# Optimization experiments

Hardware: AMD Instinct MI355X
Metric: run time of the kernel (lower is better)

Reference implementation:

```python
import jax, jax.numpy as jnp
import numpy as np

_FRAC_BITS = 8  # assumed fixed-point fractional bits for bits_quant
_SCALE = float(2 ** _FRAC_BITS)

def bits_quant(x):
    # Simulated fixed-point quantization: round to nearest multiple of 2^-8.
    return jnp.round(x * _SCALE) / _SCALE


def setup_inputs() -> dict:
    key = jax.random.key(0)
    k1, k2, k3 = jax.random.split(key, 3)
    B, D_in, D_out = 4096, 4096, 4096
    inputs = jax.random.normal(k1, (B, D_in), dtype=jnp.float32)
    w = jax.random.normal(k2, (D_in, D_out), dtype=jnp.float32) * 0.02
    b = jax.random.normal(k3, (D_out,), dtype=jnp.float32) * 0.02
    return {"inputs": inputs, "w": w, "b": b}


def reference(inputs, w, b):
    # y = bits_quant(inputs @ w) + bits_quant(b); out = bits_quant(y)
    y = bits_quant(jnp.matmul(inputs, w)) + bits_quant(b)
    return bits_quant(y)
```

## Files before the change

kernel.cpp:

```cpp
#include <hip/hip_runtime.h>
#include <math.h>

typedef __attribute__((ext_vector_type(8)))  short  short8;
typedef __attribute__((ext_vector_type(16))) float  f32x16;
typedef __attribute__((ext_vector_type(4)))  float  float4v;
typedef __attribute__((ext_vector_type(8)))  unsigned short ushort8;
typedef __attribute__((ext_vector_type(4)))  unsigned short ushort4v;

#define NDIM 4096
#define BM 256
#define BN 128
#define BK 64

#define NA_BLOCKS 2048
#define NW_BLOCKS 4096

__device__ __forceinline__ unsigned short f2bf(float f) {
  unsigned u = __builtin_bit_cast(unsigned, f);
  u += 0x7fffu + ((u >> 16) & 1u);
  return (unsigned short)(u >> 16);
}

__device__ __forceinline__ void gload_lds16(const unsigned short* g, unsigned short* l) {
  __builtin_amdgcn_global_load_lds(
      (const __attribute__((address_space(1))) void*)g,
      (__attribute__((address_space(3))) void*)l, 16, 0, 0);
}

__global__ __launch_bounds__(256)
void prep(const float* __restrict__ A, unsigned short* __restrict__ Abf,
          const float* __restrict__ W, unsigned short* __restrict__ Wt) {
  __shared__ unsigned short tile[64][72];
  const int t = threadIdx.x;
  if (blockIdx.x < NA_BLOCKS) {
    const int base   = blockIdx.x * 256 + t;
    const int stride = NA_BLOCKS * 256;
#pragma unroll
    for (int it = 0; it < 8; ++it) {
      const size_t idx = (size_t)(base + it * stride) * 4;
      float4v v = *(const float4v*)(A + idx);
      ushort4v o;
      o[0] = f2bf(v[0]); o[1] = f2bf(v[1]); o[2] = f2bf(v[2]); o[3] = f2bf(v[3]);
      *(ushort4v*)(Abf + idx) = o;
    }
  } else {
    const int b  = blockIdx.x - NA_BLOCKS;
    const int n0 = (b & 63) * 64;
    const int k0 = (b >> 6) * 64;
    const int kq = t >> 4;
    const int nc = (t & 15) * 4;
    float4v v[4];
#pragma unroll
    for (int r = 0; r < 4; ++r)
      v[r] = *(const float4v*)&W[(size_t)(k0 + kq * 4 + r) * NDIM + n0 + nc];
#pragma unroll
    for (int c = 0; c < 4; ++c) {
      ushort4v u;
#pragma unroll
      for (int r = 0; r < 4; ++r) u[r] = f2bf(v[r][c]);
      *(ushort4v*)&tile[nc + c][kq * 4] = u;
    }
    __syncthreads();
    const int n  = t >> 2;
    const int cb = (t & 3) * 16;
    unsigned short* dst = Wt + (size_t)(n0 + n) * NDIM + k0 + cb;
#pragma unroll
    for (int h = 0; h < 2; ++h) {
      ushort8 w8 = *(const ushort8*)&tile[n][cb + h * 8];
      *(ushort8*)(dst + h * 8) = w8;
    }
  }
}

__global__ __launch_bounds__(256, 2)
void gemm_bt_quant(const unsigned short* __restrict__ A,
                   const unsigned short* __restrict__ Bt,
                   const float* __restrict__ bias,
                   float* __restrict__ C) {
  __shared__ unsigned short As[BM * BK];
  __shared__ unsigned short Bs[BN * BK];

  const int tid  = threadIdx.x;
  const int lane = tid & 63;
  const int wid  = tid >> 6;
  const int wm   = (wid >> 1) * 128;
  const int wn   = (wid & 1) * 64;
  const int m0   = blockIdx.y * BM;
  const int n0   = blockIdx.x * BN;

  const int srow = tid >> 3;
  const int sc   = (tid & 7) ^ (srow & 7);
  const unsigned short* Ag = A  + (size_t)(m0 + srow) * NDIM + sc * 8;
  const unsigned short* Bg = Bt + (size_t)(n0 + srow) * NDIM + sc * 8;

  const int fr = lane & 31;
  const int fh = lane >> 5;
  const int fsw = fr & 7;

  f32x16 acc[4][2] = {};

  for (int kt = 0; kt < NDIM; kt += BK) {
#pragma unroll
    for (int p = 0; p < 8; ++p)
      gload_lds16(Ag + kt + (size_t)(p * 32) * NDIM, &As[(p * 256 + tid) * 8]);
#pragma unroll
    for (int p = 0; p < 4; ++p)
      gload_lds16(Bg + kt + (size_t)(p * 32) * NDIM, &Bs[(p * 256 + tid) * 8]);
    __syncthreads();

#pragma unroll
    for (int h = 0; h < 4; ++h) {
      const int cph = (2 * h + fh) ^ fsw;
      short8 af[4], bfr[2];
#pragma unroll
      for (int i = 0; i < 4; ++i)
        af[i] = *(const short8*)&As[(wm + i * 32 + fr) * BK + cph * 8];
#pragma unroll
      for (int j = 0; j < 2; ++j)
        bfr[j] = *(const short8*)&Bs[(wn + j * 32 + fr) * BK + cph * 8];
#pragma unroll
      for (int i = 0; i < 4; ++i)
#pragma unroll
        for (int j = 0; j < 2; ++j)
          acc[i][j] = __builtin_amdgcn_mfma_f32_32x32x16_bf16(af[i], bfr[j], acc[i][j], 0, 0, 0);
    }
    __syncthreads();
  }

  const float inv = 1.0f / 256.0f;
#pragma unroll
  for (int j = 0; j < 2; ++j) {
    const int col = n0 + wn + j * 32 + fr;
    const float qb = rintf(bias[col] * 256.0f) * inv;
#pragma unroll
    for (int i = 0; i < 4; ++i) {
      const int rb = m0 + wm + i * 32 + 4 * fh;
#pragma unroll
      for (int r = 0; r < 16; ++r) {
        const int row = rb + (r & 3) + 8 * (r >> 2);
        C[(size_t)row * NDIM + col] = rintf(acc[i][j][r] * 256.0f) * inv + qb;
      }
    }
  }
}

__global__ void gemm_fb(const float* __restrict__ A, const float* __restrict__ W,
                        const float* __restrict__ bias, float* __restrict__ C) {
  __shared__ float As[32][33], Ws[32][33];
  int tx = threadIdx.x, ty = threadIdx.y;
  int m0 = blockIdx.y * 32, n0 = blockIdx.x * 32;
  float acc[4] = {0.f, 0.f, 0.f, 0.f};
  for (int k0 = 0; k0 < NDIM; k0 += 32) {
#pragma unroll
    for (int i = 0; i < 4; ++i) {
      int r = ty + i * 8;
      As[r][tx] = A[(size_t)(m0 + r) * NDIM + k0 + tx];
      Ws[r][tx] = W[(size_t)(k0 + r) * NDIM + n0 + tx];
    }
    __syncthreads();
#pragma unroll
    for (int k = 0; k < 32; ++k) {
      float wv = Ws[k][tx];
#pragma unroll
      for (int i = 0; i < 4; ++i) acc[i] += As[ty + i * 8][k] * wv;
    }
    __syncthreads();
  }
  float qb = rintf(bias[n0 + tx] * 256.0f) * (1.0f / 256.0f);
#pragma unroll
  for (int i = 0; i < 4; ++i)
    C[(size_t)(m0 + ty + i * 8) * NDIM + n0 + tx] =
        rintf(acc[i] * 256.0f) * (1.0f / 256.0f) + qb;
}

extern "C" void kernel_launch(void* const* d_in, const int* in_sizes, int n_in,
                              void* d_out, int out_size, void* d_ws, size_t ws_size,
                              hipStream_t stream) {
  const float* A    = (const float*)d_in[0];
  const float* W    = (const float*)d_in[1];
  const float* bias = (const float*)d_in[2];
  float* C = (float*)d_out;
  const size_t nElem = (size_t)NDIM * NDIM;

  if (ws_size >= nElem * 4) {
    unsigned short* Abf = (unsigned short*)d_ws;
    unsigned short* Wt  = Abf + nElem;
    prep<<<NA_BLOCKS + NW_BLOCKS, 256, 0, stream>>>(A, Abf, W, Wt);
    gemm_bt_quant<<<dim3(NDIM / BN, NDIM / BM), 256, 0, stream>>>(Abf, Wt, bias, C);
  } else {
    gemm_fb<<<dim3(128, 128), dim3(32, 8), 0, stream>>>(A, W, bias, C);
  }
}
```

Baseline: 304.3 us.

## Triple-buffer LDS tiles with async global-to-LDS prefetch two stages ahead

Replaces the single-buffered load/sync/compute loop with a three-slot LDS ring. Tile t+2 is issued via global_load_lds while tile t is computed, and the loop waits on vmcnt with one barrier per iteration. This is meant to hide global memory latency behind MFMA work. The larger LDS footprint (about 144KB) lowers occupancy to one block per CU, so launch_bounds is changed to match.

```diff
diff --git a/kernel.cpp b/kernel.cpp
--- a/kernel.cpp
+++ b/kernel.cpp
@@ -11,6 +11,8 @@
 #define BM 256
 #define BN 128
 #define BK 64
+#define T_TILES (NDIM / BK)
+#define BUF_USH (BM * BK + BN * BK)
 
 #define NA_BLOCKS 2048
 #define NW_BLOCKS 4096
@@ -72,13 +74,12 @@
   }
 }
 
-__global__ __launch_bounds__(256, 2)
+__global__ __launch_bounds__(256, 1)
 void gemm_bt_quant(const unsigned short* __restrict__ A,
                    const unsigned short* __restrict__ Bt,
                    const float* __restrict__ bias,
                    float* __restrict__ C) {
-  __shared__ unsigned short As[BM * BK];
-  __shared__ unsigned short Bs[BN * BK];
+  __shared__ unsigned short lds[3 * BUF_USH];
 
   const int tid  = threadIdx.x;
   const int lane = tid & 63;
@@ -93,38 +94,58 @@
   const unsigned short* Ag = A  + (size_t)(m0 + srow) * NDIM + sc * 8;
   const unsigned short* Bg = Bt + (size_t)(n0 + srow) * NDIM + sc * 8;
 
-  const int fr = lane & 31;
-  const int fh = lane >> 5;
+  const int fr  = lane & 31;
+  const int fh  = lane >> 5;
   const int fsw = fr & 7;
 
   f32x16 acc[4][2] = {};
 
-  for (int kt = 0; kt < NDIM; kt += BK) {
+  auto stage = [&](int k, int buf) {
+    unsigned short* Asb = &lds[buf * BUF_USH];
+    unsigned short* Bsb = Asb + BM * BK;
+    const int ko = k * BK;
 #pragma unroll
     for (int p = 0; p < 8; ++p)
-      gload_lds16(Ag + kt + (size_t)(p * 32) * NDIM, &As[(p * 256 + tid) * 8]);
+      gload_lds16(Ag + ko + (size_t)(p * 32) * NDIM, &Asb[(p * 256 + tid) * 8]);
 #pragma unroll
     for (int p = 0; p < 4; ++p)
-      gload_lds16(Bg + kt + (size_t)(p * 32) * NDIM, &Bs[(p * 256 + tid) * 8]);
-    __syncthreads();
-
+      gload_lds16(Bg + ko + (size_t)(p * 32) * NDIM, &Bsb[(p * 256 + tid) * 8]);
+  };
+
+  stage(0, 0);
+  stage(1, 1);
+
+  int b = 0, b2 = 2;
+  for (int t = 0; t < T_TILES; ++t) {
+    if (t < T_TILES - 1)
+      asm volatile("s_waitcnt vmcnt(12)" ::: "memory");
+    else
+      asm volatile("s_waitcnt vmcnt(0)" ::: "memory");
+    __builtin_amdgcn_s_barrier();
+    __builtin_amdgcn_sched_barrier(0);
+
+    if (t + 2 < T_TILES) stage(t + 2, b2);
+
+    const unsigned short* Asb = &lds[b * BUF_USH];
+    const unsigned short* Bsb = Asb + BM * BK;
 #pragma unroll
     for (int h = 0; h < 4; ++h) {
       const int cph = (2 * h + fh) ^ fsw;
       short8 af[4], bfr[2];
 #pragma unroll
       for (int i = 0; i < 4; ++i)
-        af[i] = *(const short8*)&As[(wm + i * 32 + fr) * BK + cph * 8];
+        af[i] = *(const short8*)&Asb[(wm + i * 32 + fr) * BK + cph * 8];
 #pragma unroll
       for (int j = 0; j < 2; ++j)
-        bfr[j] = *(const short8*)&Bs[(wn + j * 32 + fr) * BK + cph * 8];
+        bfr[j] = *(const short8*)&Bsb[(wn + j * 32 + fr) * BK + cph * 8];
 #pragma unroll
       for (int i = 0; i < 4; ++i)
 #pragma unroll
         for (int j = 0; j < 2; ++j)
           acc[i][j] = __builtin_amdgcn_mfma_f32_32x32x16_bf16(af[i], bfr[j], acc[i][j], 0, 0, 0);
     }
-    __syncthreads();
+    b  = (b  + 1 == 3) ? 0 : b  + 1;
+    b2 = (b2 + 1 == 3) ? 0 : b2 + 1;
   }
 
   const float inv = 1.0f / 256.0f;
```

New measurement: 314.3 us. +3.3%, slower.

## Pipeline GEMM with 256x256 tiles, 8 waves and rotating LDS buffers

Applied to the files above, without the earlier changes.

The GEMM moves to 256x256 block tiles with 512 threads (8 waves) and a rotating multi-slot LDS ring: A uses 5 half-tile slots and B uses 4, so the next tiles' global-to-LDS loads are issued while MFMAs run on the current ones. It replaces the load/sync/compute/sync loop with explicit vmcnt waits, barriers, sched_barrier and setprio. A block-index swizzle is added to improve L2 reuse. The larger LDS footprint (about 144KB) and register use may lower occupancy, and the hand-tuned waitcnt counts carry a risk of race conditions.

```diff
diff --git a/kernel.cpp b/kernel.cpp
--- a/kernel.cpp
+++ b/kernel.cpp
@@ -9,8 +9,11 @@
 
 #define NDIM 4096
 #define BM 256
-#define BN 128
+#define BN 256
 #define BK 64
+#define T_TILES (NDIM / BK)
+#define HALF_USH 8192
+#define B_BASE   (5 * HALF_USH)
 
 #define NA_BLOCKS 2048
 #define NW_BLOCKS 4096
@@ -72,73 +75,122 @@
   }
 }
 
-__global__ __launch_bounds__(256, 2)
+__global__ __launch_bounds__(512, 2)
 void gemm_bt_quant(const unsigned short* __restrict__ A,
                    const unsigned short* __restrict__ Bt,
                    const float* __restrict__ bias,
                    float* __restrict__ C) {
-  __shared__ unsigned short As[BM * BK];
-  __shared__ unsigned short Bs[BN * BK];
+  __shared__ unsigned short lds[9 * HALF_USH];
 
   const int tid  = threadIdx.x;
   const int lane = tid & 63;
   const int wid  = tid >> 6;
-  const int wm   = (wid >> 1) * 128;
-  const int wn   = (wid & 1) * 64;
-  const int m0   = blockIdx.y * BM;
-  const int n0   = blockIdx.x * BN;
+  const int wr   = wid >> 2;
+  const int wc   = wid & 3;
+  const int hb   = wc >> 1;
+  const int bnr  = (wc & 1) * 64;
+
+  const int bid  = blockIdx.y * 16 + blockIdx.x;
+  const int swz  = (bid & 7) * 32 + (bid >> 3);
+  const int m0   = (swz >> 4) * BM;
+  const int n0   = (swz & 15) * BN;
 
   const int srow = tid >> 3;
   const int sc   = (tid & 7) ^ (srow & 7);
   const unsigned short* Ag = A  + (size_t)(m0 + srow) * NDIM + sc * 8;
   const unsigned short* Bg = Bt + (size_t)(n0 + srow) * NDIM + sc * 8;
 
-  const int fr = lane & 31;
-  const int fh = lane >> 5;
+  const int fr  = lane & 31;
+  const int fh  = lane >> 5;
   const int fsw = fr & 7;
 
+  auto stageA = [&](int tt, int ha, int slot) {
+    unsigned short* dst = &lds[slot * HALF_USH];
+    const unsigned short* g = Ag + (size_t)(ha * 128) * NDIM + tt * 64;
+    gload_lds16(g,                       &dst[tid * 8]);
+    gload_lds16(g + (size_t)64 * NDIM,   &dst[(512 + tid) * 8]);
+  };
+  auto stageB = [&](int tt, int hb2, int slot) {
+    unsigned short* dst = &lds[B_BASE + slot * HALF_USH];
+    const unsigned short* g = Bg + (size_t)(hb2 * 128) * NDIM + tt * 64;
+    gload_lds16(g,                       &dst[tid * 8]);
+    gload_lds16(g + (size_t)64 * NDIM,   &dst[(512 + tid) * 8]);
+  };
+
   f32x16 acc[4][2] = {};
 
-  for (int kt = 0; kt < NDIM; kt += BK) {
-#pragma unroll
-    for (int p = 0; p < 8; ++p)
-      gload_lds16(Ag + kt + (size_t)(p * 32) * NDIM, &As[(p * 256 + tid) * 8]);
-#pragma unroll
-    for (int p = 0; p < 4; ++p)
-      gload_lds16(Bg + kt + (size_t)(p * 32) * NDIM, &Bs[(p * 256 + tid) * 8]);
-    __syncthreads();
-
-#pragma unroll
-    for (int h = 0; h < 4; ++h) {
-      const int cph = (2 * h + fh) ^ fsw;
-      short8 af[4], bfr[2];
-#pragma unroll
-      for (int i = 0; i < 4; ++i)
-        af[i] = *(const short8*)&As[(wm + i * 32 + fr) * BK + cph * 8];
-#pragma unroll
-      for (int j = 0; j < 2; ++j)
-        bfr[j] = *(const short8*)&Bs[(wn + j * 32 + fr) * BK + cph * 8];
-#pragma unroll
-      for (int i = 0; i < 4; ++i)
+  stageB(0, 0, 0);
+  stageB(0, 1, 1);
+  stageA(0, 0, 0);
+  stageA(0, 1, 1);
+  stageB(1, 0, 2);
+  stageB(1, 1, 3);
+
+  int raA = wr;
+  int rbB = hb;
+  int sA0 = 2, sA1 = 3;
+  int sB0 = 0, sB1 = 1;
+
+  for (int t = 0; t < T_TILES; ++t) {
+    const unsigned short* Ah = &lds[raA * HALF_USH];
+    const unsigned short* Bh = &lds[B_BASE + rbB * HALF_USH];
+    short8 bk[2][4];
+#pragma unroll
+    for (int p = 0; p < 4; ++p) {
+      if (p == 0) {
+        if (t < T_TILES - 1) asm volatile("s_waitcnt vmcnt(4)" ::: "memory");
+        else                 asm volatile("s_waitcnt vmcnt(0)" ::: "memory");
+      }
+      __builtin_amdgcn_s_barrier();
+      __builtin_amdgcn_sched_barrier(0);
+
+      if (p == 0) {
 #pragma unroll
         for (int j = 0; j < 2; ++j)
-          acc[i][j] = __builtin_amdgcn_mfma_f32_32x32x16_bf16(af[i], bfr[j], acc[i][j], 0, 0, 0);
-    }
-    __syncthreads();
+#pragma unroll
+          for (int h = 0; h < 4; ++h)
+            bk[j][h] = *(const short8*)&Bh[(bnr + j * 32 + fr) * 64 + ((2 * h + fh) ^ fsw) * 8];
+      }
+      short8 af[4];
+#pragma unroll
+      for (int h = 0; h < 4; ++h)
+        af[h] = *(const short8*)&Ah[(p * 32 + fr) * 64 + ((2 * h + fh) ^ fsw) * 8];
+
+      if (p == 0 && t + 1 < T_TILES) stageA(t + 1, 0, sA0);
+      if (p == 1 && t + 1 < T_TILES) stageA(t + 1, 1, sA1);
+      if (p == 2 && t + 2 < T_TILES) stageB(t + 2, 0, sB0);
+      if (p == 3 && t + 2 < T_TILES) stageB(t + 2, 1, sB1);
+
+      asm volatile("s_waitcnt lgkmcnt(0)" ::: "memory");
+      __builtin_amdgcn_sched_barrier(0);
+      __builtin_amdgcn_s_setprio(1);
+#pragma unroll
+      for (int h = 0; h < 4; ++h)
+#pragma unroll
+        for (int j = 0; j < 2; ++j)
+          acc[p][j] = __builtin_amdgcn_mfma_f32_32x32x16_bf16(af[h], bk[j][h], acc[p][j], 0, 0, 0);
+      __builtin_amdgcn_s_setprio(0);
+    }
+    raA += 2; if (raA >= 5) raA -= 5;
+    sA0 += 2; if (sA0 >= 5) sA0 -= 5;
+    sA1 += 2; if (sA1 >= 5) sA1 -= 5;
+    rbB = (rbB + 2) & 3;
+    sB0 = (sB0 + 2) & 3;
+    sB1 = (sB1 + 2) & 3;
   }
 
   const float inv = 1.0f / 256.0f;
 #pragma unroll
   for (int j = 0; j < 2; ++j) {
-    const int col = n0 + wn + j * 32 + fr;
+    const int col = n0 + wc * 64 + j * 32 + fr;
     const float qb = rintf(bias[col] * 256.0f) * inv;
 #pragma unroll
-    for (int i = 0; i < 4; ++i) {
-      const int rb = m0 + wm + i * 32 + 4 * fh;
+    for (int p = 0; p < 4; ++p) {
+      const int rb = m0 + wr * 128 + p * 32 + 4 * fh;
 #pragma unroll
       for (int r = 0; r < 16; ++r) {
         const int row = rb + (r & 3) + 8 * (r >> 2);
-        C[(size_t)row * NDIM + col] = rintf(acc[i][j][r] * 256.0f) * inv + qb;
+        C[(size_t)row * NDIM + col] = rintf(acc[p][j][r] * 256.0f) * inv + qb;
       }
     }
   }
@@ -186,7 +238,7 @@
     unsigned short* Abf = (unsigned short*)d_ws;
     unsigned short* Wt  = Abf + nElem;
     prep<<<NA_BLOCKS + NW_BLOCKS, 256, 0, stream>>>(A, Abf, W, Wt);
-    gemm_bt_quant<<<dim3(NDIM / BN, NDIM / BM), 256, 0, stream>>>(Abf, Wt, bias, C);
+    gemm_bt_quant<<<dim3(16, 16), 512, 0, stream>>>(Abf, Wt, bias, C);
   } else {
     gemm_fb<<<dim3(128, 128), dim3(32, 8), 0, stream>>>(A, W, bias, C);
   }
```

Measured after the change: 298.4 us. About the same (-1.9%).
